# Kernel optimization log

Measured on AMD Instinct MI355X. Metric: run time of the kernel, lower is better.

Reference implementation:

```python
import jax, jax.numpy as jnp
import numpy as np

NUM_EXPERTS = 8
TOP_K = 2
N_EMBD = 1024
SEQ = 2048
BATCH = 1
BLOCK = 128
D_FFN = ((4 * N_EMBD // TOP_K) + BLOCK - 1) // BLOCK * BLOCK  # 2048


def setup_inputs() -> dict:
    key = jax.random.key(0)
    k_x, k_r, k_w1, k_w2 = jax.random.split(key, 4)
    x = jax.random.normal(k_x, (BATCH, SEQ, N_EMBD), dtype=jnp.float32)
    # nn.Linear(n_embd, num_experts, bias=False) -> weight [E, D]
    w_router = jax.random.normal(k_r, (NUM_EXPERTS, N_EMBD), dtype=jnp.float32) * 0.02
    # trunc_normal std=0.02 approximated by clipped normal
    w1 = jnp.clip(jax.random.normal(k_w1, (N_EMBD, D_FFN * NUM_EXPERTS), dtype=jnp.float32) * 0.02, -0.06, 0.06)
    w2 = jnp.clip(jax.random.normal(k_w2, (D_FFN * NUM_EXPERTS, N_EMBD), dtype=jnp.float32) * 0.02, -0.06, 0.06)
    return {"x": x, "w_router": w_router, "w1": w1, "w2": w2}


def reference(x, w_router, w1, w2):
    B, S, D = x.shape
    E = w_router.shape[0]
    d_ffn = w1.shape[1] // E
    xf = x.reshape(-1, D)                      # [N, D]
    N = xf.shape[0]

    # --- routing (softmax in fp32, top-k, renormalize) ---
    logits = xf @ w_router.T                   # [N, E]
    probs = jax.nn.softmax(logits.astype(jnp.float32), axis=-1)
    topw, sel = jax.lax.top_k(probs, TOP_K)    # [N, k]
    topw = topw / jnp.sum(topw, axis=-1, keepdims=True)
    topw = topw.astype(x.dtype)

    # dense per-token gate matrix [N, E]; zero for unselected experts, so the
    # dense grouped-GEMM below computes exactly the routed-expert math.
    gates = jnp.zeros((N, E), dtype=x.dtype).at[jnp.arange(N)[:, None], sel].set(topw)

    w1r = w1.reshape(D, E, d_ffn)              # expert e uses columns e*d_ffn:(e+1)*d_ffn
    w2r = w2.reshape(E, d_ffn, D)

    out = jnp.zeros_like(xf)
    for e in range(E):                         # small fixed expert count
        h = jax.nn.gelu(xf @ w1r[:, e, :], approximate=False)  # torch F.gelu = exact erf
        out = out + gates[:, e:e + 1] * (h @ w2r[e])
    return out.reshape(B, S, D)
```

## Files before the change

### kernel.cpp

```cpp
#include <hip/hip_runtime.h>

typedef short bf16x8 __attribute__((ext_vector_type(8)));
typedef float f32x4 __attribute__((ext_vector_type(4)));
typedef unsigned short u16;
typedef unsigned int u32;

#define N_TOK 2048
#define D_EMB 1024
#define D_FFNC 2048
#define N_EXP 8

__device__ __forceinline__ u16 f2bf(float f) {
    u32 u = __builtin_bit_cast(u32, f);
    u32 r = (u + 0x7fffu + ((u >> 16) & 1u)) >> 16;
    return (u16)r;
}

__device__ __forceinline__ void gl_lds16(const void* g, void* l) {
    __builtin_amdgcn_global_load_lds((const __attribute__((address_space(1))) u32*)g,
                                     (__attribute__((address_space(3))) u32*)l, 16, 0, 0);
}

__global__ __launch_bounds__(256) void k_router(const float* __restrict__ x,
                                                const float* __restrict__ wr,
                                                u16* __restrict__ xb,
                                                int* __restrict__ eids,
                                                float* __restrict__ gate2) {
    int lane = threadIdx.x & 63;
    int wv = threadIdx.x >> 6;
    int t = blockIdx.x * 4 + wv;
    const float* xp = x + (size_t)t * D_EMB;
    float p[N_EXP];
#pragma unroll
    for (int e = 0; e < N_EXP; e++) p[e] = 0.f;
#pragma unroll
    for (int i = 0; i < 4; i++) {
        int idx = (i * 64 + lane) * 4;
        float4 v = *reinterpret_cast<const float4*>(xp + idx);
        ushort4 o;
        o.x = f2bf(v.x); o.y = f2bf(v.y); o.z = f2bf(v.z); o.w = f2bf(v.w);
        *reinterpret_cast<ushort4*>(xb + (size_t)t * D_EMB + idx) = o;
#pragma unroll
        for (int e = 0; e < N_EXP; e++) {
            float4 w = *reinterpret_cast<const float4*>(wr + e * D_EMB + idx);
            p[e] += v.x * w.x + v.y * w.y + v.z * w.z + v.w * w.w;
        }
    }
#pragma unroll
    for (int off = 32; off; off >>= 1) {
#pragma unroll
        for (int e = 0; e < N_EXP; e++) p[e] += __shfl_xor(p[e], off);
    }
    float mx = p[0];
#pragma unroll
    for (int e = 1; e < N_EXP; e++) mx = fmaxf(mx, p[e]);
    float pr[N_EXP];
#pragma unroll
    for (int e = 0; e < N_EXP; e++) pr[e] = expf(p[e] - mx);
    int e1 = 0; float v1 = pr[0];
#pragma unroll
    for (int e = 1; e < N_EXP; e++) { if (pr[e] > v1) { v1 = pr[e]; e1 = e; } }
    int e2 = -1; float v2 = -1.f;
#pragma unroll
    for (int e = 0; e < N_EXP; e++) { if (e != e1 && pr[e] > v2) { v2 = pr[e]; e2 = e; } }
    if (lane == 0) {
        float inv = 1.f / (v1 + v2);
        eids[t * 2] = e1; eids[t * 2 + 1] = e2;
        gate2[t * 2] = v1 * inv; gate2[t * 2 + 1] = v2 * inv;
    }
}

__global__ __launch_bounds__(256) void k_transpose2(const float* __restrict__ w1,
                                                    const float* __restrict__ w2,
                                                    u16* __restrict__ w1t,
                                                    u16* __restrict__ w2t) {
    __shared__ float tl[64][65];
    const float* in; u16* out; int R, C, c0, r0;
    if (blockIdx.z == 0) { in = w1; out = w1t; R = 1024; C = 16384; c0 = blockIdx.x * 64; r0 = blockIdx.y * 64; }
    else                 { in = w2; out = w2t; R = 16384; C = 1024; c0 = blockIdx.y * 64; r0 = blockIdx.x * 64; }
    int tid = threadIdx.x;
    int rr = tid >> 4, c4 = (tid & 15) * 4;
#pragma unroll
    for (int i = 0; i < 4; i++) {
        int r = rr + i * 16;
        float4 v = *reinterpret_cast<const float4*>(in + (size_t)(r0 + r) * C + c0 + c4);
        tl[r][c4] = v.x; tl[r][c4 + 1] = v.y; tl[r][c4 + 2] = v.z; tl[r][c4 + 3] = v.w;
    }
    __syncthreads();
    int k4 = (tid & 15) * 4;
#pragma unroll
    for (int i = 0; i < 4; i++) {
        int cc = rr + i * 16;
        ushort4 o;
        o.x = f2bf(tl[k4][cc]); o.y = f2bf(tl[k4 + 1][cc]);
        o.z = f2bf(tl[k4 + 2][cc]); o.w = f2bf(tl[k4 + 3][cc]);
        *reinterpret_cast<ushort4*>(out + (size_t)(c0 + cc) * R + r0 + k4) = o;
    }
}

__global__ __launch_bounds__(1024) void k_build(const int* __restrict__ eids,
                                                const float* __restrict__ gate2,
                                                int* __restrict__ cnt, int* __restrict__ basep,
                                                int* __restrict__ rowmeta, float* __restrict__ rowgate) {
    __shared__ int scnt[8], sbase[8], sfill[8];
    int tid = threadIdx.x;
    if (tid < 8) { scnt[tid] = 0; sfill[tid] = 0; }
    __syncthreads();
    for (int t = tid; t < N_TOK; t += 1024) {
        atomicAdd(&scnt[eids[2 * t]], 1);
        atomicAdd(&scnt[eids[2 * t + 1]], 1);
    }
    __syncthreads();
    if (tid == 0) { int s = 0; for (int e = 0; e < 8; e++) { sbase[e] = s; s += scnt[e]; } }
    __syncthreads();
    if (tid < 8) { cnt[tid] = scnt[tid]; basep[tid] = sbase[tid]; }
    for (int t = tid; t < N_TOK; t += 1024) {
#pragma unroll
        for (int s = 0; s < 2; s++) {
            int e = eids[2 * t + s];
            int pos = atomicAdd(&sfill[e], 1);
            int g = sbase[e] + pos;
            rowmeta[g] = t | (s << 16);
            rowgate[g] = gate2[2 * t + s];
        }
    }
}

__global__ __launch_bounds__(256) void k_zero(float* __restrict__ p) {
    int idx = blockIdx.x * 256 + threadIdx.x;
    *reinterpret_cast<float4*>(p + (size_t)idx * 4) = (float4){0.f, 0.f, 0.f, 0.f};
}

__global__ __launch_bounds__(256) void k_gemm1(const u16* __restrict__ xb,
                                               const u16* __restrict__ w1t,
                                               const int* __restrict__ cnt,
                                               const int* __restrict__ basep,
                                               const int* __restrict__ rowmeta,
                                               u16* __restrict__ hbuf) {
    int e = blockIdx.z;
    int nrows = cnt[e];
    int mt = blockIdx.x, nt = blockIdx.y;
    if (mt * 128 >= nrows) return;
    int b0 = basep[e];
    __shared__ u16 lA[2][128 * 64];
    __shared__ u16 lB[2][128 * 64];
    int tid = threadIdx.x, lane = tid & 63, wv = tid >> 6;
    int srow8 = lane >> 3, c8 = lane & 7;
    int csw = (c8 ^ srow8) * 16;
    const char* xbB = (const char*)xb;
    const char* w1tB = (const char*)w1t;
    size_t asrc[4], bsrc[4];
    int ldso[4];
#pragma unroll
    for (int i = 0; i < 4; i++) {
        int r = wv * 32 + i * 8 + srow8;
        int g = mt * 128 + r;
        int tok = (g < nrows) ? (rowmeta[b0 + g] & 0xffff) : (rowmeta[b0] & 0xffff);
        asrc[i] = (size_t)tok * 2048 + csw;
        int colg = nt * 128 + r;
        bsrc[i] = (size_t)(e * 2048 + colg) * 2048 + csw;
        ldso[i] = (wv * 32 + i * 8) * 64;
    }
    f32x4 acc[4][4];
#pragma unroll
    for (int m = 0; m < 4; m++)
#pragma unroll
        for (int n = 0; n < 4; n++) acc[m][n] = (f32x4){0.f, 0.f, 0.f, 0.f};
    int wr = (wv >> 1) * 64, wc = (wv & 1) * 64;
    int lr = lane & 15, kg = lane >> 4;

    auto stage = [&](int buf, int kt) {
        size_t ko = (size_t)kt * 128;
#pragma unroll
        for (int i = 0; i < 4; i++) {
            gl_lds16(xbB + asrc[i] + ko, lA[buf] + ldso[i]);
            gl_lds16(w1tB + bsrc[i] + ko, lB[buf] + ldso[i]);
        }
    };
    stage(0, 0);
    for (int kt = 0; kt < 16; kt++) {
        if (kt < 15) {
            stage((kt + 1) & 1, kt + 1);
            asm volatile("s_waitcnt vmcnt(8)" ::: "memory");
        } else {
            asm volatile("s_waitcnt vmcnt(0)" ::: "memory");
        }
        __builtin_amdgcn_s_barrier();
        const u16* la = lA[kt & 1];
        const u16* lb = lB[kt & 1];
#pragma unroll
        for (int h2 = 0; h2 < 2; h2++) {
            bf16x8 af[4], bfr[4];
#pragma unroll
            for (int m = 0; m < 4; m++)
                af[m] = *(const bf16x8*)(la + (wr + m * 16 + lr) * 64 + (((h2 * 4 + kg) ^ (lr & 7)) * 8));
#pragma unroll
            for (int n = 0; n < 4; n++)
                bfr[n] = *(const bf16x8*)(lb + (wc + n * 16 + lr) * 64 + (((h2 * 4 + kg) ^ (lr & 7)) * 8));
#pragma unroll
            for (int m = 0; m < 4; m++)
#pragma unroll
                for (int n = 0; n < 4; n++)
                    acc[m][n] = __builtin_amdgcn_mfma_f32_16x16x32_bf16(af[m], bfr[n], acc[m][n], 0, 0, 0);
        }
        __builtin_amdgcn_s_barrier();
    }
#pragma unroll
    for (int m = 0; m < 4; m++) {
        int rbase = wr + m * 16 + kg * 4;
#pragma unroll
        for (int j = 0; j < 4; j++) {
            int r = mt * 128 + rbase + j;
            if (r < nrows) {
                u16* hp = hbuf + (size_t)(b0 + r) * D_FFNC + nt * 128 + wc + lr;
#pragma unroll
                for (int n = 0; n < 4; n++) {
                    float v = acc[m][n][j];
                    v = 0.5f * v * (1.f + erff(v * 0.70710678118654752f));
                    hp[n * 16] = f2bf(v);
                }
            }
        }
    }
}

__global__ __launch_bounds__(256) void k_gemm2(const u16* __restrict__ hbuf,
                                               const u16* __restrict__ w2t,
                                               const int* __restrict__ cnt,
                                               const int* __restrict__ basep,
                                               const int* __restrict__ rowmeta,
                                               const float* __restrict__ rowgate,
                                               float* __restrict__ out) {
    int e = blockIdx.z;
    int nrows = cnt[e];
    int mt = blockIdx.x, nt = blockIdx.y;
    if (mt * 128 >= nrows) return;
    int b0 = basep[e];
    __shared__ u16 lA[2][128 * 64];
    __shared__ u16 lB[2][128 * 64];
    int tid = threadIdx.x, lane = tid & 63, wv = tid >> 6;
    int srow8 = lane >> 3, c8 = lane & 7;
    int csw = (c8 ^ srow8) * 16;
    const char* hB = (const char*)hbuf;
    const char* w2tB = (const char*)w2t;
    size_t asrc[4], bsrc[4];
    int ldso[4];
#pragma unroll
    for (int i = 0; i < 4; i++) {
        int r = wv * 32 + i * 8 + srow8;
        int g = mt * 128 + r;
        int hr = b0 + ((g < nrows) ? g : (nrows - 1));
        asrc[i] = (size_t)hr * 4096 + csw;
        int colg = nt * 128 + r;
        bsrc[i] = (size_t)colg * 32768 + (size_t)e * 4096 + csw;
        ldso[i] = (wv * 32 + i * 8) * 64;
    }
    f32x4 acc[4][4];
#pragma unroll
    for (int m = 0; m < 4; m++)
#pragma unroll
        for (int n = 0; n < 4; n++) acc[m][n] = (f32x4){0.f, 0.f, 0.f, 0.f};
    int wr = (wv >> 1) * 64, wc = (wv & 1) * 64;
    int lr = lane & 15, kg = lane >> 4;

    auto stage = [&](int buf, int kt) {
        size_t ko = (size_t)kt * 128;
#pragma unroll
        for (int i = 0; i < 4; i++) {
            gl_lds16(hB + asrc[i] + ko, lA[buf] + ldso[i]);
            gl_lds16(w2tB + bsrc[i] + ko, lB[buf] + ldso[i]);
        }
    };
    stage(0, 0);
    for (int kt = 0; kt < 32; kt++) {
        if (kt < 31) {
            stage((kt + 1) & 1, kt + 1);
            asm volatile("s_waitcnt vmcnt(8)" ::: "memory");
        } else {
            asm volatile("s_waitcnt vmcnt(0)" ::: "memory");
        }
        __builtin_amdgcn_s_barrier();
        const u16* la = lA[kt & 1];
        const u16* lb = lB[kt & 1];
#pragma unroll
        for (int h2 = 0; h2 < 2; h2++) {
            bf16x8 af[4], bfr[4];
#pragma unroll
            for (int m = 0; m < 4; m++)
                af[m] = *(const bf16x8*)(la + (wr + m * 16 + lr) * 64 + (((h2 * 4 + kg) ^ (lr & 7)) * 8));
#pragma unroll
            for (int n = 0; n < 4; n++)
                bfr[n] = *(const bf16x8*)(lb + (wc + n * 16 + lr) * 64 + (((h2 * 4 + kg) ^ (lr & 7)) * 8));
#pragma unroll
            for (int m = 0; m < 4; m++)
#pragma unroll
                for (int n = 0; n < 4; n++)
                    acc[m][n] = __builtin_amdgcn_mfma_f32_16x16x32_bf16(af[m], bfr[n], acc[m][n], 0, 0, 0);
        }
        __builtin_amdgcn_s_barrier();
    }
#pragma unroll
    for (int m = 0; m < 4; m++) {
        int rbase = wr + m * 16 + kg * 4;
#pragma unroll
        for (int j = 0; j < 4; j++) {
            int r = mt * 128 + rbase + j;
            if (r < nrows) {
                int tok = rowmeta[b0 + r] & 0xffff;
                float gw = rowgate[b0 + r];
                float* op = out + (size_t)tok * D_EMB + nt * 128 + wc + lr;
#pragma unroll
                for (int n = 0; n < 4; n++) atomicAdd(&op[n * 16], gw * acc[m][n][j]);
            }
        }
    }
}

extern "C" void kernel_launch(void* const* d_in, const int* in_sizes, int n_in,
                              void* d_out, int out_size, void* d_ws, size_t ws_size,
                              hipStream_t stream) {
    const float* x = (const float*)d_in[0];
    const float* wrt = (const float*)d_in[1];
    const float* w1 = (const float*)d_in[2];
    const float* w2 = (const float*)d_in[3];
    float* out = (float*)d_out;
    char* ws = (char*)d_ws;
    size_t off = 0;
    auto alloc = [&](size_t b) { void* p = ws + off; off += (b + 255) & ~(size_t)255; return p; };
    u16* xb = (u16*)alloc((size_t)N_TOK * D_EMB * 2);
    u16* w1t = (u16*)alloc((size_t)16384 * 1024 * 2);
    u16* w2t = (u16*)alloc((size_t)16384 * 1024 * 2);
    u16* hbuf = (u16*)alloc((size_t)4096 * D_FFNC * 2);
    int* eids = (int*)alloc(N_TOK * 2 * 4);
    float* gate2 = (float*)alloc(N_TOK * 2 * 4);
    int* rowmeta = (int*)alloc(4096 * 4);
    float* rowgate = (float*)alloc(4096 * 4);
    int* cnt = (int*)alloc(64);
    int* basep = (int*)alloc(64);

    k_router<<<512, 256, 0, stream>>>(x, wrt, xb, eids, gate2);
    k_transpose2<<<dim3(256, 16, 2), 256, 0, stream>>>(w1, w2, w1t, w2t);
    k_build<<<1, 1024, 0, stream>>>(eids, gate2, cnt, basep, rowmeta, rowgate);
    k_zero<<<2048, 256, 0, stream>>>(out);
    k_gemm1<<<dim3(16, 16, 8), 256, 0, stream>>>(xb, w1t, cnt, basep, rowmeta, hbuf);
    k_gemm2<<<dim3(16, 8, 8), 256, 0, stream>>>(hbuf, w2t, cnt, basep, rowmeta, rowgate, out);
}
```

Baseline: 383.4 us.

## Replace LDS-staged expert GEMMs with direct global-to-register MFMA loads

Both expert GEMM kernels drop the shared-memory double-buffered staging (global_load_lds plus barriers). Each wave now loads its MFMA fragments straight from global memory into registers with a two-deep software prefetch. The block tile changes from 128x128 to 64 rows x 256 columns, with each wave owning a 64x64 subtile, and the grids are adjusted to match. This removes LDS traffic and barrier stalls, but the four waves in a block no longer share A-tile loads. Global accesses become strided 16-byte-per-lane reads that rely on L1/L2 for reuse. The final prefetch also reads one step past K, landing in adjacent workspace memory.

```diff
diff --git a/kernel.cpp b/kernel.cpp
--- a/kernel.cpp
+++ b/kernel.cpp
@@ -14,11 +14,6 @@
     u32 u = __builtin_bit_cast(u32, f);
     u32 r = (u + 0x7fffu + ((u >> 16) & 1u)) >> 16;
     return (u16)r;
-}
-
-__device__ __forceinline__ void gl_lds16(const void* g, void* l) {
-    __builtin_amdgcn_global_load_lds((const __attribute__((address_space(1))) u32*)g,
-                                     (__attribute__((address_space(3))) u32*)l, 16, 0, 0);
 }
 
 __global__ __launch_bounds__(256) void k_router(const float* __restrict__ x,
@@ -139,80 +134,66 @@
                                                u16* __restrict__ hbuf) {
     int e = blockIdx.z;
     int nrows = cnt[e];
-    int mt = blockIdx.x, nt = blockIdx.y;
-    if (mt * 128 >= nrows) return;
+    int mt = blockIdx.x;
+    if (mt * 64 >= nrows) return;
     int b0 = basep[e];
-    __shared__ u16 lA[2][128 * 64];
-    __shared__ u16 lB[2][128 * 64];
-    int tid = threadIdx.x, lane = tid & 63, wv = tid >> 6;
-    int srow8 = lane >> 3, c8 = lane & 7;
-    int csw = (c8 ^ srow8) * 16;
-    const char* xbB = (const char*)xb;
-    const char* w1tB = (const char*)w1t;
-    size_t asrc[4], bsrc[4];
-    int ldso[4];
-#pragma unroll
-    for (int i = 0; i < 4; i++) {
-        int r = wv * 32 + i * 8 + srow8;
-        int g = mt * 128 + r;
-        int tok = (g < nrows) ? (rowmeta[b0 + g] & 0xffff) : (rowmeta[b0] & 0xffff);
-        asrc[i] = (size_t)tok * 2048 + csw;
-        int colg = nt * 128 + r;
-        bsrc[i] = (size_t)(e * 2048 + colg) * 2048 + csw;
-        ldso[i] = (wv * 32 + i * 8) * 64;
-    }
+    int lane = threadIdx.x & 63, wv = threadIdx.x >> 6;
+    int lr = lane & 15, kq = lane >> 4;
+    int col0 = blockIdx.y * 256 + wv * 64;
+
+    const char* aB[4];
+    const char* bB[4];
+#pragma unroll
+    for (int m = 0; m < 4; m++) {
+        int g = mt * 64 + m * 16 + lr;
+        int gc = (g < nrows) ? g : (nrows - 1);
+        int tok = rowmeta[b0 + gc] & 0xffff;
+        aB[m] = (const char*)xb + (size_t)tok * 2048 + kq * 16;
+    }
+#pragma unroll
+    for (int n = 0; n < 4; n++) {
+        int colg = e * 2048 + col0 + n * 16 + lr;
+        bB[n] = (const char*)w1t + (size_t)colg * 2048 + kq * 16;
+    }
+
     f32x4 acc[4][4];
 #pragma unroll
     for (int m = 0; m < 4; m++)
 #pragma unroll
         for (int n = 0; n < 4; n++) acc[m][n] = (f32x4){0.f, 0.f, 0.f, 0.f};
-    int wr = (wv >> 1) * 64, wc = (wv & 1) * 64;
-    int lr = lane & 15, kg = lane >> 4;
-
-    auto stage = [&](int buf, int kt) {
-        size_t ko = (size_t)kt * 128;
-#pragma unroll
-        for (int i = 0; i < 4; i++) {
-            gl_lds16(xbB + asrc[i] + ko, lA[buf] + ldso[i]);
-            gl_lds16(w1tB + bsrc[i] + ko, lB[buf] + ldso[i]);
-        }
+
+    bf16x8 a0[4], b0f[4], a1[4], b1f[4];
+    auto ld = [&](bf16x8* va, bf16x8* vb, int kt) {
+        size_t o = (size_t)kt * 64;
+#pragma unroll
+        for (int m = 0; m < 4; m++) va[m] = *(const bf16x8*)(aB[m] + o);
+#pragma unroll
+        for (int n = 0; n < 4; n++) vb[n] = *(const bf16x8*)(bB[n] + o);
     };
-    stage(0, 0);
-    for (int kt = 0; kt < 16; kt++) {
-        if (kt < 15) {
-            stage((kt + 1) & 1, kt + 1);
-            asm volatile("s_waitcnt vmcnt(8)" ::: "memory");
-        } else {
-            asm volatile("s_waitcnt vmcnt(0)" ::: "memory");
-        }
-        __builtin_amdgcn_s_barrier();
-        const u16* la = lA[kt & 1];
-        const u16* lb = lB[kt & 1];
-#pragma unroll
-        for (int h2 = 0; h2 < 2; h2++) {
-            bf16x8 af[4], bfr[4];
-#pragma unroll
-            for (int m = 0; m < 4; m++)
-                af[m] = *(const bf16x8*)(la + (wr + m * 16 + lr) * 64 + (((h2 * 4 + kg) ^ (lr & 7)) * 8));
+    auto mm = [&](bf16x8* va, bf16x8* vb) {
+#pragma unroll
+        for (int m = 0; m < 4; m++)
 #pragma unroll
             for (int n = 0; n < 4; n++)
-                bfr[n] = *(const bf16x8*)(lb + (wc + n * 16 + lr) * 64 + (((h2 * 4 + kg) ^ (lr & 7)) * 8));
-#pragma unroll
-            for (int m = 0; m < 4; m++)
-#pragma unroll
-                for (int n = 0; n < 4; n++)
-                    acc[m][n] = __builtin_amdgcn_mfma_f32_16x16x32_bf16(af[m], bfr[n], acc[m][n], 0, 0, 0);
-        }
-        __builtin_amdgcn_s_barrier();
-    }
+                acc[m][n] = __builtin_amdgcn_mfma_f32_16x16x32_bf16(va[m], vb[n], acc[m][n], 0, 0, 0);
+    };
+
+    ld(a0, b0f, 0);
+    for (int kt = 0; kt < 32; kt += 2) {
+        ld(a1, b1f, kt + 1);
+        mm(a0, b0f);
+        ld(a0, b0f, kt + 2);
+        mm(a1, b1f);
+    }
+
 #pragma unroll
     for (int m = 0; m < 4; m++) {
-        int rbase = wr + m * 16 + kg * 4;
+        int rbase = mt * 64 + m * 16 + kq * 4;
 #pragma unroll
         for (int j = 0; j < 4; j++) {
-            int r = mt * 128 + rbase + j;
+            int r = rbase + j;
             if (r < nrows) {
-                u16* hp = hbuf + (size_t)(b0 + r) * D_FFNC + nt * 128 + wc + lr;
+                u16* hp = hbuf + (size_t)(b0 + r) * D_FFNC + col0 + lr;
 #pragma unroll
                 for (int n = 0; n < 4; n++) {
                     float v = acc[m][n][j];
@@ -233,82 +214,67 @@
                                                float* __restrict__ out) {
     int e = blockIdx.z;
     int nrows = cnt[e];
-    int mt = blockIdx.x, nt = blockIdx.y;
-    if (mt * 128 >= nrows) return;
+    int mt = blockIdx.x;
+    if (mt * 64 >= nrows) return;
     int b0 = basep[e];
-    __shared__ u16 lA[2][128 * 64];
-    __shared__ u16 lB[2][128 * 64];
-    int tid = threadIdx.x, lane = tid & 63, wv = tid >> 6;
-    int srow8 = lane >> 3, c8 = lane & 7;
-    int csw = (c8 ^ srow8) * 16;
-    const char* hB = (const char*)hbuf;
-    const char* w2tB = (const char*)w2t;
-    size_t asrc[4], bsrc[4];
-    int ldso[4];
-#pragma unroll
-    for (int i = 0; i < 4; i++) {
-        int r = wv * 32 + i * 8 + srow8;
-        int g = mt * 128 + r;
-        int hr = b0 + ((g < nrows) ? g : (nrows - 1));
-        asrc[i] = (size_t)hr * 4096 + csw;
-        int colg = nt * 128 + r;
-        bsrc[i] = (size_t)colg * 32768 + (size_t)e * 4096 + csw;
-        ldso[i] = (wv * 32 + i * 8) * 64;
-    }
+    int lane = threadIdx.x & 63, wv = threadIdx.x >> 6;
+    int lr = lane & 15, kq = lane >> 4;
+    int col0 = blockIdx.y * 256 + wv * 64;
+
+    const char* aB[4];
+    const char* bB[4];
+#pragma unroll
+    for (int m = 0; m < 4; m++) {
+        int g = mt * 64 + m * 16 + lr;
+        int gc = (g < nrows) ? g : (nrows - 1);
+        aB[m] = (const char*)hbuf + (size_t)(b0 + gc) * 4096 + kq * 16;
+    }
+#pragma unroll
+    for (int n = 0; n < 4; n++) {
+        int col = col0 + n * 16 + lr;
+        bB[n] = (const char*)w2t + (size_t)col * 32768 + (size_t)e * 4096 + kq * 16;
+    }
+
     f32x4 acc[4][4];
 #pragma unroll
     for (int m = 0; m < 4; m++)
 #pragma unroll
         for (int n = 0; n < 4; n++) acc[m][n] = (f32x4){0.f, 0.f, 0.f, 0.f};
-    int wr = (wv >> 1) * 64, wc = (wv & 1) * 64;
-    int lr = lane & 15, kg = lane >> 4;
-
-    auto stage = [&](int buf, int kt) {
-        size_t ko = (size_t)kt * 128;
-#pragma unroll
-        for (int i = 0; i < 4; i++) {
-            gl_lds16(hB + asrc[i] + ko, lA[buf] + ldso[i]);
-            gl_lds16(w2tB + bsrc[i] + ko, lB[buf] + ldso[i]);
-        }
+
+    bf16x8 a0[4], b0f[4], a1[4], b1f[4];
+    auto ld = [&](bf16x8* va, bf16x8* vb, int kt) {
+        size_t o = (size_t)kt * 64;
+#pragma unroll
+        for (int m = 0; m < 4; m++) va[m] = *(const bf16x8*)(aB[m] + o);
+#pragma unroll
+        for (int n = 0; n < 4; n++) vb[n] = *(const bf16x8*)(bB[n] + o);
     };
-    stage(0, 0);
-    for (int kt = 0; kt < 32; kt++) {
-        if (kt < 31) {
-            stage((kt + 1) & 1, kt + 1);
-            asm volatile("s_waitcnt vmcnt(8)" ::: "memory");
-        } else {
-            asm volatile("s_waitcnt vmcnt(0)" ::: "memory");
-        }
-        __builtin_amdgcn_s_barrier();
-        const u16* la = lA[kt & 1];
-        const u16* lb = lB[kt & 1];
-#pragma unroll
-        for (int h2 = 0; h2 < 2; h2++) {
-            bf16x8 af[4], bfr[4];
-#pragma unroll
-            for (int m = 0; m < 4; m++)
-                af[m] = *(const bf16x8*)(la + (wr + m * 16 + lr) * 64 + (((h2 * 4 + kg) ^ (lr & 7)) * 8));
+    auto mm = [&](bf16x8* va, bf16x8* vb) {
+#pragma unroll
+        for (int m = 0; m < 4; m++)
 #pragma unroll
             for (int n = 0; n < 4; n++)
-                bfr[n] = *(const bf16x8*)(lb + (wc + n * 16 + lr) * 64 + (((h2 * 4 + kg) ^ (lr & 7)) * 8));
-#pragma unroll
-            for (int m = 0; m < 4; m++)
-#pragma unroll
-                for (int n = 0; n < 4; n++)
-                    acc[m][n] = __builtin_amdgcn_mfma_f32_16x16x32_bf16(af[m], bfr[n], acc[m][n], 0, 0, 0);
-        }
-        __builtin_amdgcn_s_barrier();
-    }
+                acc[m][n] = __builtin_amdgcn_mfma_f32_16x16x32_bf16(va[m], vb[n], acc[m][n], 0, 0, 0);
+    };
+
+    ld(a0, b0f, 0);
+    for (int kt = 0; kt < 64; kt += 2) {
+        ld(a1, b1f, kt + 1);
+        mm(a0, b0f);
+        ld(a0, b0f, kt + 2);
+        mm(a1, b1f);
+    }
+
 #pragma unroll
     for (int m = 0; m < 4; m++) {
-        int rbase = wr + m * 16 + kg * 4;
+        int rbase = mt * 64 + m * 16 + kq * 4;
 #pragma unroll
         for (int j = 0; j < 4; j++) {
-            int r = mt * 128 + rbase + j;
+            int r = rbase + j;
             if (r < nrows) {
                 int tok = rowmeta[b0 + r] & 0xffff;
                 float gw = rowgate[b0 + r];
-                float* op = out + (size_t)tok * D_EMB + nt * 128 + wc + lr;
+                float* op = out + (size_t)tok * D_EMB + col0 + lr;
 #pragma unroll
                 for (int n = 0; n < 4; n++) atomicAdd(&op[n * 16], gw * acc[m][n][j]);
             }
@@ -342,6 +308,6 @@
     k_transpose2<<<dim3(256, 16, 2), 256, 0, stream>>>(w1, w2, w1t, w2t);
     k_build<<<1, 1024, 0, stream>>>(eids, gate2, cnt, basep, rowmeta, rowgate);
     k_zero<<<2048, 256, 0, stream>>>(out);
-    k_gemm1<<<dim3(16, 16, 8), 256, 0, stream>>>(xb, w1t, cnt, basep, rowmeta, hbuf);
-    k_gemm2<<<dim3(16, 8, 8), 256, 0, stream>>>(hbuf, w2t, cnt, basep, rowmeta, rowgate, out);
-}
+    k_gemm1<<<dim3(32, 8, 8), 256, 0, stream>>>(xb, w1t, cnt, basep, rowmeta, hbuf);
+    k_gemm2<<<dim3(32, 4, 8), 256, 0, stream>>>(hbuf, w2t, cnt, basep, rowmeta, rowgate, out);
+}
```

Result: slower. 681.0 us (+77.6%).
